# Kernel tuning notes

Hardware: AMD Instinct MI355X
Metric: run time of the kernel (lower is better)

Reference implementation:

```python
import jax, jax.numpy as jnp
import numpy as np

B, T, C, H = 2, 2048, 1024, 16
D = C // H  # head dim = 64
EPS = 1e-6  # kernel adds 1e-6 to softmax denominator


def setup_inputs() -> dict:
    key = jax.random.key(0)
    k1, k2, k3, k4, k5 = jax.random.split(key, 5)
    s = 1.0 / np.sqrt(C)
    return {
        "x": jax.random.normal(k1, (B, T, C), dtype=jnp.float32),
        "w_attn": jax.random.normal(k2, (3 * C, C), dtype=jnp.float32) * s,
        "b_attn": jax.random.normal(k3, (3 * C,), dtype=jnp.float32) * 0.02,
        "w_proj": jax.random.normal(k4, (C, C), dtype=jnp.float32) * s,
        "b_proj": jax.random.normal(k5, (C,), dtype=jnp.float32) * 0.02,
    }


def reference(x, w_attn, b_attn, w_proj, b_proj):
    b, t, c = x.shape
    qkv = x @ w_attn.T + b_attn                      # [B,T,3C]
    q, k, v = jnp.split(qkv, 3, axis=2)
    # [B,T,C] -> [B,H,T,D]
    q = q.reshape(b, t, H, D).transpose(0, 2, 1, 3)
    k = k.reshape(b, t, H, D).transpose(0, 2, 1, 3)
    v = v.reshape(b, t, H, D).transpose(0, 2, 1, 3)
    scale = 1.0 / np.sqrt(D)
    att = jnp.einsum("bhid,bhjd->bhij", q, k) * scale  # [B,H,T,T]
    causal = jnp.tril(jnp.ones((t, t), dtype=bool))
    att = jnp.where(causal, att, -jnp.inf)
    # softmax matching the HIP kernel: denom has +1e-6
    m = jnp.max(att, axis=-1, keepdims=True)
    e = jnp.exp(att - m)                             # masked entries -> 0
    p = e / (jnp.sum(e, axis=-1, keepdims=True) + EPS)
    y = jnp.einsum("bhij,bhjd->bhid", p, v)          # [B,H,T,D]
    y = y.transpose(0, 2, 1, 3).reshape(b, t, c)     # [B,T,C]
    return y @ w_proj.T + b_proj
```

## Files before the change

### kernel.cpp

```cpp
#include <hip/hip_runtime.h>

#define B_ 2
#define T_ 2048
#define C_ 1024
#define H_ 16
#define D_ 64

typedef __bf16 bf16x8 __attribute__((ext_vector_type(8)));
typedef float f32x4 __attribute__((ext_vector_type(4)));

__device__ __forceinline__ unsigned short f2bf(float f) {
  unsigned u = __float_as_uint(f);
  unsigned r = (u + 0x7fffu + ((u >> 16) & 1u)) >> 16;
  return (unsigned short)r;
}

__device__ __forceinline__ float exp2_hw(float x) {
  float r;
  asm("v_exp_f32 %0, %1" : "=v"(r) : "v"(x));
  return r;
}

#define NX 1048576
#define NWA 786432
#define NWP 262144
__global__ __launch_bounds__(256) void convert_all(
    const float* __restrict__ x, const float* __restrict__ wa,
    const float* __restrict__ wp, unsigned short* __restrict__ xb,
    unsigned short* __restrict__ wab, unsigned short* __restrict__ wpb) {
  int i = blockIdx.x * 256 + threadIdx.x;
  const float* s; unsigned short* d; int j;
  if (i < NX)            { s = x;  d = xb;  j = i; }
  else if (i < NX + NWA) { s = wa; d = wab; j = i - NX; }
  else                   { s = wp; d = wpb; j = i - NX - NWA; }
  float4 v = ((const float4*)s)[j];
  ushort4 u;
  u.x = f2bf(v.x); u.y = f2bf(v.y); u.z = f2bf(v.z); u.w = f2bf(v.w);
  ((ushort4*)d)[j] = u;
}

__global__ __launch_bounds__(256) void gemm_bt(
    const unsigned short* __restrict__ A,
    const unsigned short* __restrict__ Bm,
    const float* __restrict__ bias,
    int M, int N, int K, int mode,
    float* __restrict__ outf,
    unsigned short* __restrict__ qb,
    unsigned short* __restrict__ kb,
    unsigned short* __restrict__ vb) {
  __shared__ unsigned short As[128 * 64];
  __shared__ unsigned short Bs[128 * 64];

  const int tid  = threadIdx.x;
  const int lane = tid & 63;
  const int wave = tid >> 6;
  const int quad = lane >> 4;
  const int l16  = lane & 15;
  const int q4   = quad * 4;

  const int bm = blockIdx.y * 128;
  const int bn = blockIdx.x * 128;
  const int wm = (wave >> 1) * 64;
  const int wn = (wave & 1) * 64;

  f32x4 acc[4][4] = {};

  const int srow8 = lane >> 3;
  const int scol  = ((lane & 7) ^ srow8) * 8;
  const int srow  = wave * 8 + srow8;

  for (int k0 = 0; k0 < K; k0 += 64) {
#pragma unroll
    for (int c = 0; c < 4; ++c) {
      const int r = c * 32 + srow;
      const unsigned short* ga = A  + (size_t)(bm + r) * K + (k0 + scol);
      const unsigned short* gb = Bm + (size_t)(bn + r) * K + (k0 + scol);
      unsigned short* la = &As[(c * 32 + wave * 8) * 64];
      unsigned short* lb = &Bs[(c * 32 + wave * 8) * 64];
      __builtin_amdgcn_global_load_lds(
          (__attribute__((address_space(1))) unsigned int*)ga,
          (__attribute__((address_space(3))) unsigned int*)la, 16, 0, 0);
      __builtin_amdgcn_global_load_lds(
          (__attribute__((address_space(1))) unsigned int*)gb,
          (__attribute__((address_space(3))) unsigned int*)lb, 16, 0, 0);
    }
    __syncthreads();
#pragma unroll
    for (int ks = 0; ks < 2; ++ks) {
      bf16x8 af[4], bfr[4];
#pragma unroll
      for (int i = 0; i < 4; ++i)
        af[i] = *(const bf16x8*)&As[(wm + i * 16 + l16) * 64 +
                                    (((ks * 4 + quad) ^ (l16 & 7)) * 8)];
#pragma unroll
      for (int j = 0; j < 4; ++j)
        bfr[j] = *(const bf16x8*)&Bs[(wn + j * 16 + l16) * 64 +
                                     (((ks * 4 + quad) ^ (l16 & 7)) * 8)];
#pragma unroll
      for (int i = 0; i < 4; ++i)
#pragma unroll
        for (int j = 0; j < 4; ++j)
          acc[i][j] = __builtin_amdgcn_mfma_f32_16x16x32_bf16(af[i], bfr[j], acc[i][j], 0, 0, 0);
    }
    __syncthreads();
  }

#pragma unroll
  for (int j = 0; j < 4; ++j) {
    const int gn = bn + wn + j * 16 + l16;
    const float bv = bias[gn];
    if (mode == 0) {
#pragma unroll
      for (int i = 0; i < 4; ++i)
#pragma unroll
        for (int r = 0; r < 4; ++r) {
          const int gm = bm + wm + i * 16 + q4 + r;
          outf[(size_t)gm * N + gn] = acc[i][j][r] + bv;
        }
    } else {
      const int which = gn >> 10;
      const int cc = gn & 1023;
      const int h = cc >> 6, d = cc & 63;
      if (which == 2) {
#pragma unroll
        for (int i = 0; i < 4; ++i) {
          const int gm0 = bm + wm + i * 16 + q4;
          const int b = gm0 >> 11, t0 = gm0 & 2047;
          ushort4 u;
          u.x = f2bf(acc[i][j][0] + bv);
          u.y = f2bf(acc[i][j][1] + bv);
          u.z = f2bf(acc[i][j][2] + bv);
          u.w = f2bf(acc[i][j][3] + bv);
          *(ushort4*)&vb[(((size_t)(b * H_ + h) * D_) + d) * T_ + t0] = u;
        }
      } else {
        const float sc = (which == 0) ? 0.18033688011112042f : 1.0f;
        unsigned short* dst = (which == 0) ? qb : kb;
#pragma unroll
        for (int i = 0; i < 4; ++i)
#pragma unroll
          for (int r = 0; r < 4; ++r) {
            const int gm = bm + wm + i * 16 + q4 + r;
            const int b = gm >> 11, t = gm & 2047;
            dst[(((size_t)(b * H_ + h) * T_) + t) * D_ + d] = f2bf((acc[i][j][r] + bv) * sc);
          }
      }
    }
  }
}

__global__ __launch_bounds__(256, 2) void attn_mfma(
    const unsigned short* __restrict__ Qb,
    const unsigned short* __restrict__ Kb,
    const unsigned short* __restrict__ Vtg,
    unsigned short* __restrict__ Yb,
    unsigned short* __restrict__ op,
    float* __restrict__ lp) {
  __shared__ unsigned short Ks[2][64 * 64];
  __shared__ unsigned short Vt[2][64 * 64];
  __shared__ unsigned short Pw[4][32 * 64];

  const int tid  = threadIdx.x;
  const int lane = tid & 63;
  const int wave = tid >> 6;
  const int quad = lane >> 4;
  const int l16  = lane & 15;
  const int q4   = quad * 4;
  const int sw   = (l16 & 7);

  const int id = blockIdx.x;
  const int bh = id / 40;
  const int w  = id - bh * 40;
  int qt, chunk, nsplits;
  if (w < 4)       { qt = w;                 chunk = 0;            nsplits = 1; }
  else if (w < 12) { qt = 4 + ((w - 4) >> 1); chunk = (w - 4) & 1;  nsplits = 2; }
  else if (w < 24) { qt = 8 + (w - 12) / 3;  chunk = (w - 12) % 3; nsplits = 3; }
  else             { qt = 12 + ((w - 24) >> 2); chunk = (w - 24) & 3; nsplits = 4; }

  const int tiles_total = 2 * qt + 2;
  const int tpc = (tiles_total + nsplits - 1) / nsplits;
  const int t0 = chunk * tpc;
  const int t1 = min(t0 + tpc, tiles_total);

  const int b = bh >> 4, h = bh & 15;
  const size_t base = (size_t)bh * T_ * D_;
  const int wq = qt * 128 + wave * 32;
  const int wt1 = min(t1, (wq + 95) >> 6);

  bf16x8 qf[2][2];
#pragma unroll
  for (int nt = 0; nt < 2; ++nt)
#pragma unroll
    for (int ks = 0; ks < 2; ++ks)
      qf[nt][ks] = *(const bf16x8*)(Qb + base + (size_t)(wq + nt * 16 + l16) * 64 +
                                    ks * 32 + quad * 8);

  f32x4 o[4][2] = {};
  float l2[2] = {0.f, 0.f};

  const int srow8 = lane >> 3;
  const int satom = ((lane & 7) ^ srow8) * 8;

#define STAGE_KV(KT, BI)                                                       \
  do {                                                                         \
    const int kt0s = (KT) * 64;                                                \
    _Pragma("unroll")                                                          \
    for (int c = 0; c < 2; ++c) {                                              \
      const int row = wave * 16 + c * 8 + srow8;                               \
      const unsigned short* gk = Kb + base + (size_t)(kt0s + row) * 64 + satom;\
      const unsigned short* gv = Vtg + base + (size_t)row * T_ + kt0s + satom; \
      unsigned short* lk = &Ks[BI][(wave * 16 + c * 8) * 64];                  \
      unsigned short* lv = &Vt[BI][(wave * 16 + c * 8) * 64];                  \
      __builtin_amdgcn_global_load_lds(                                        \
          (__attribute__((address_space(1))) unsigned int*)gk,                 \
          (__attribute__((address_space(3))) unsigned int*)lk, 16, 0, 0);      \
      __builtin_amdgcn_global_load_lds(                                        \
          (__attribute__((address_space(1))) unsigned int*)gv,                 \
          (__attribute__((address_space(3))) unsigned int*)lv, 16, 0, 0);      \
    }                                                                          \
  } while (0)

  STAGE_KV(t0, 0);
  int cur = 0;

  for (int kt = t0; kt < t1; ++kt) {
    const int kt0 = kt * 64;
    __syncthreads();
    if (kt + 1 < t1) STAGE_KV(kt + 1, cur ^ 1);

    if (kt < wt1) {
      f32x4 s[4][2] = {};
#pragma unroll
      for (int ks = 0; ks < 2; ++ks) {
        bf16x8 kf[4];
#pragma unroll
        for (int mt = 0; mt < 4; ++mt)
          kf[mt] = *(const bf16x8*)&Ks[cur][(mt * 16 + l16) * 64 +
                                           (((ks * 4 + quad) ^ sw) * 8)];
        __builtin_amdgcn_s_setprio(1);
#pragma unroll
        for (int mt = 0; mt < 4; ++mt)
#pragma unroll
          for (int nt = 0; nt < 2; ++nt)
            s[mt][nt] = __builtin_amdgcn_mfma_f32_16x16x32_bf16(kf[mt], qf[nt][ks],
                                                                s[mt][nt], 0, 0, 0);
        __builtin_amdgcn_s_setprio(0);
      }
      if (kt0 + 63 > wq) {
#pragma unroll
        for (int mt = 0; mt < 4; ++mt)
#pragma unroll
          for (int nt = 0; nt < 2; ++nt)
#pragma unroll
            for (int r = 0; r < 4; ++r)
              if (kt0 + mt * 16 + q4 + r > wq + nt * 16 + l16) s[mt][nt][r] = -1e30f;
      }
#pragma unroll
      for (int nt = 0; nt < 2; ++nt) {
        float ps = 0.f;
#pragma unroll
        for (int mt = 0; mt < 4; ++mt) {
          float p0 = exp2_hw(s[mt][nt][0]);
          float p1 = exp2_hw(s[mt][nt][1]);
          float p2 = exp2_hw(s[mt][nt][2]);
          float p3 = exp2_hw(s[mt][nt][3]);
          ps += (p0 + p1) + (p2 + p3);
          unsigned lo, hi;
          asm("v_cvt_pk_bf16_f32 %0, %1, %2" : "=v"(lo) : "v"(p0), "v"(p1));
          asm("v_cvt_pk_bf16_f32 %0, %1, %2" : "=v"(hi) : "v"(p2), "v"(p3));
          uint2 pk; pk.x = lo; pk.y = hi;
          const int atom = (2 * mt + (quad >> 1)) ^ sw;
          *(uint2*)&Pw[wave][(nt * 16 + l16) * 64 + atom * 8 + (quad & 1) * 4] = pk;
        }
        l2[nt] += ps;
      }
#pragma unroll
      for (int ks = 0; ks < 2; ++ks) {
        bf16x8 vf[4], pf[2];
#pragma unroll
        for (int dt = 0; dt < 4; ++dt)
          vf[dt] = *(const bf16x8*)&Vt[cur][(dt * 16 + l16) * 64 +
                                           (((ks * 4 + quad) ^ sw) * 8)];
#pragma unroll
        for (int nt = 0; nt < 2; ++nt)
          pf[nt] = *(const bf16x8*)&Pw[wave][(nt * 16 + l16) * 64 +
                                            (((ks * 4 + quad) ^ sw) * 8)];
        __builtin_amdgcn_s_setprio(1);
#pragma unroll
        for (int dt = 0; dt < 4; ++dt)
#pragma unroll
          for (int nt = 0; nt < 2; ++nt)
            o[dt][nt] = __builtin_amdgcn_mfma_f32_16x16x32_bf16(vf[dt], pf[nt],
                                                                o[dt][nt], 0, 0, 0);
        __builtin_amdgcn_s_setprio(0);
      }
    }
    cur ^= 1;
  }
#undef STAGE_KV

#pragma unroll
  for (int nt = 0; nt < 2; ++nt) {
    float l = l2[nt];
    l += __shfl_xor(l, 16);
    l += __shfl_xor(l, 32);
    const int qloc = wave * 32 + nt * 16 + l16;
    if (nsplits == 1) {
      const float inv = 1.f / (l + 1e-6f);
      const int q = qt * 128 + qloc;
#pragma unroll
      for (int dt = 0; dt < 4; ++dt) {
        ushort4 u;
        u.x = f2bf(o[dt][nt][0] * inv);
        u.y = f2bf(o[dt][nt][1] * inv);
        u.z = f2bf(o[dt][nt][2] * inv);
        u.w = f2bf(o[dt][nt][3] * inv);
        *(ushort4*)&Yb[((size_t)(b * T_ + q)) * C_ + h * 64 + dt * 16 + q4] = u;
      }
    } else {
      if (quad == 0) lp[(size_t)id * 128 + qloc] = l;
#pragma unroll
      for (int dt = 0; dt < 4; ++dt) {
        ushort4 u;
        u.x = f2bf(o[dt][nt][0]);
        u.y = f2bf(o[dt][nt][1]);
        u.z = f2bf(o[dt][nt][2]);
        u.w = f2bf(o[dt][nt][3]);
        *(ushort4*)&op[(size_t)id * 8192 + (size_t)qloc * 64 + dt * 16 + q4] = u;
      }
    }
  }
}

__global__ __launch_bounds__(256) void attn_combine(
    const unsigned short* __restrict__ op, const float* __restrict__ lp,
    unsigned short* __restrict__ Yb) {
  const int cb = blockIdx.x;
  const int bh = cb / 12;
  const int qi = cb - bh * 12;
  const int qt = 4 + qi;
  int nsplits, pfx;
  if (qt < 8)       { nsplits = 2; pfx = 4 + 2 * (qt - 4); }
  else if (qt < 12) { nsplits = 3; pfx = 12 + 3 * (qt - 8); }
  else              { nsplits = 4; pfx = 24 + 4 * (qt - 12); }
  const int slot0 = bh * 40 + pfx;

  const int t = threadIdx.x;
  const int qloc = t >> 1;
  const int d0 = (t & 1) * 32;

  float l = 1e-6f;
  float acc[32];
#pragma unroll
  for (int i = 0; i < 32; ++i) acc[i] = 0.f;
  for (int s = 0; s < nsplits; ++s) {
    l += lp[(size_t)(slot0 + s) * 128 + qloc];
    const uint4* src = (const uint4*)(op + (size_t)(slot0 + s) * 8192 +
                                      (size_t)qloc * 64 + d0);
#pragma unroll
    for (int c = 0; c < 4; ++c) {
      uint4 v = src[c];
      acc[c*8+0] += __uint_as_float(v.x << 16);
      acc[c*8+1] += __uint_as_float(v.x & 0xffff0000u);
      acc[c*8+2] += __uint_as_float(v.y << 16);
      acc[c*8+3] += __uint_as_float(v.y & 0xffff0000u);
      acc[c*8+4] += __uint_as_float(v.z << 16);
      acc[c*8+5] += __uint_as_float(v.z & 0xffff0000u);
      acc[c*8+6] += __uint_as_float(v.w << 16);
      acc[c*8+7] += __uint_as_float(v.w & 0xffff0000u);
    }
  }
  const float inv = 1.f / l;
  const int b = bh >> 4, h = bh & 15;
  const int q = qt * 128 + qloc;
  uint4* dst = (uint4*)(Yb + ((size_t)(b * T_ + q)) * C_ + h * 64 + d0);
#pragma unroll
  for (int c = 0; c < 4; ++c) {
    uint4 v;
    v.x = (unsigned)f2bf(acc[c*8+0] * inv) | ((unsigned)f2bf(acc[c*8+1] * inv) << 16);
    v.y = (unsigned)f2bf(acc[c*8+2] * inv) | ((unsigned)f2bf(acc[c*8+3] * inv) << 16);
    v.z = (unsigned)f2bf(acc[c*8+4] * inv) | ((unsigned)f2bf(acc[c*8+5] * inv) << 16);
    v.w = (unsigned)f2bf(acc[c*8+6] * inv) | ((unsigned)f2bf(acc[c*8+7] * inv) << 16);
    dst[c] = v;
  }
}

extern "C" void kernel_launch(void* const* d_in, const int* in_sizes, int n_in,
                              void* d_out, int out_size, void* d_ws, size_t ws_size,
                              hipStream_t stream) {
  const float* x      = (const float*)d_in[0];
  const float* w_attn = (const float*)d_in[1];
  const float* b_attn = (const float*)d_in[2];
  const float* w_proj = (const float*)d_in[3];
  const float* b_proj = (const float*)d_in[4];
  float* out = (float*)d_out;

  char* ws = (char*)d_ws;
  unsigned short* xb  = (unsigned short*)ws;  ws += (size_t)4096 * 1024 * 2;
  unsigned short* wab = (unsigned short*)ws;  ws += (size_t)3072 * 1024 * 2;
  unsigned short* wpb = (unsigned short*)ws;  ws += (size_t)1024 * 1024 * 2;
  unsigned short* qb  = (unsigned short*)ws;  ws += (size_t)B_ * H_ * T_ * D_ * 2;
  unsigned short* kb  = (unsigned short*)ws;  ws += (size_t)B_ * H_ * T_ * D_ * 2;
  unsigned short* vb  = (unsigned short*)ws;  ws += (size_t)B_ * H_ * T_ * D_ * 2;
  unsigned short* yb  = (unsigned short*)ws;  ws += (size_t)4096 * 1024 * 2;
  unsigned short* op  = (unsigned short*)ws;  ws += (size_t)1280 * 128 * 64 * 2;
  float*          lp  = (float*)ws;           ws += (size_t)1280 * 128 * 4;
  (void)ws_size; (void)in_sizes; (void)n_in; (void)out_size;

  convert_all<<<8192, 256, 0, stream>>>(x, w_attn, w_proj, xb, wab, wpb);

  gemm_bt<<<dim3(24, 32), 256, 0, stream>>>(xb, wab, b_attn, 4096, 3072, 1024, 1,
                                            nullptr, qb, kb, vb);
  attn_mfma<<<1280, 256, 0, stream>>>(qb, kb, vb, yb, op, lp);
  attn_combine<<<384, 256, 0, stream>>>(op, lp, yb);
  gemm_bt<<<dim3(8, 32), 256, 0, stream>>>(yb, wpb, b_proj, 4096, 1024, 1024, 0,
                                           out, nullptr, nullptr, nullptr);
}
```

Baseline: 185.8 us.

## Add 256x256 double-buffered QKV GEMM with direct global-to-LDS loads

Replaces the 128x128 QKV projection GEMM with a dedicated 512-thread kernel that computes 256x256 tiles. It double-buffers LDS, stages tiles with global_load_lds, and splits each K-step into four phases that interleave the next tile's loads with MFMA work, using barriers and priority hints. Blocks are remapped so neighbouring blocks share tiles. The aim is more data reuse per block and less time waiting on loads, but the grid drops to 192 blocks (fewer than the CU count) and each block uses much more LDS and registers, which limits occupancy.

```diff
diff --git a/kernel.cpp b/kernel.cpp
--- a/kernel.cpp
+++ b/kernel.cpp
@@ -39,15 +39,159 @@
   ((ushort4*)d)[j] = u;
 }
 
+__global__ __launch_bounds__(512, 2) void gemm_qkv_256(
+    const unsigned short* __restrict__ A,
+    const unsigned short* __restrict__ Bm,
+    const float* __restrict__ bias,
+    unsigned short* __restrict__ qb,
+    unsigned short* __restrict__ kb,
+    unsigned short* __restrict__ vb) {
+  __shared__ unsigned short As[2][256 * 64];
+  __shared__ unsigned short Bs[2][256 * 64];
+
+  const int tid  = threadIdx.x;
+  const int lane = tid & 63;
+  const int wave = tid >> 6;
+  const int quad = lane >> 4;
+  const int l16  = lane & 15;
+  const int q4   = quad * 4;
+  const int wr   = wave >> 2;
+  const int wc   = wave & 3;
+
+  const int id0 = blockIdx.x;
+  const int nid = (id0 & 7) * 24 + (id0 >> 3);
+  const int bm = (nid / 12) * 256;
+  const int bn = (nid % 12) * 256;
+
+  f32x4 acc[8][4] = {};
+  bf16x8 af[2][4], bf[2][2];
+
+  const int srow8 = lane >> 3;
+  const int satom = ((lane & 7) ^ srow8) * 8;
+
+#define STG64(G, LPTR, GROW, KCOL)                                             \
+  do {                                                                         \
+    const unsigned short* g_ = (G) + (size_t)(GROW) * 1024 + (KCOL) + satom;   \
+    __builtin_amdgcn_global_load_lds(                                          \
+        (__attribute__((address_space(1))) unsigned int*)g_,                   \
+        (__attribute__((address_space(3))) unsigned int*)(LPTR), 16, 0, 0);    \
+  } while (0)
+
+#define STG_HALF(G, LS, BUF, HH, KCOL, RB)                                     \
+  do {                                                                         \
+    STG64(G, &LS[BUF][((HH) * 128 + wave * 8) * 64],                           \
+          (RB) + (HH) * 128 + wave * 8 + srow8, KCOL);                         \
+    STG64(G, &LS[BUF][((HH) * 128 + 64 + wave * 8) * 64],                      \
+          (RB) + (HH) * 128 + 64 + wave * 8 + srow8, KCOL);                    \
+  } while (0)
+
+#define LOAD_AF(BUF, IH)                                                       \
+  _Pragma("unroll") for (int ks_ = 0; ks_ < 2; ++ks_)                          \
+  _Pragma("unroll") for (int i_ = 0; i_ < 4; ++i_)                             \
+    af[ks_][i_] = *(const bf16x8*)&As[BUF][(wr * 128 + (IH) * 64 + i_ * 16 +   \
+                                            l16) * 64 +                        \
+                                           (((ks_ * 4 + quad) ^ (l16 & 7)) * 8)]
+
+#define LOAD_BF(BUF, JH)                                                       \
+  _Pragma("unroll") for (int ks_ = 0; ks_ < 2; ++ks_)                          \
+  _Pragma("unroll") for (int j_ = 0; j_ < 2; ++j_)                             \
+    bf[ks_][j_] = *(const bf16x8*)&Bs[BUF][(wc * 64 + (JH) * 32 + j_ * 16 +    \
+                                            l16) * 64 +                        \
+                                           (((ks_ * 4 + quad) ^ (l16 & 7)) * 8)]
+
+#define MFMA_Q(IH, JH)                                                         \
+  _Pragma("unroll") for (int ks_ = 0; ks_ < 2; ++ks_)                          \
+  _Pragma("unroll") for (int i_ = 0; i_ < 4; ++i_)                             \
+  _Pragma("unroll") for (int j_ = 0; j_ < 2; ++j_)                             \
+    acc[(IH) * 4 + i_][(JH) * 2 + j_] = __builtin_amdgcn_mfma_f32_16x16x32_bf16( \
+        af[ks_][i_], bf[ks_][j_], acc[(IH) * 4 + i_][(JH) * 2 + j_], 0, 0, 0)
+
+#define PHASE(BUF, IH, JH, LA, LB, STGSTMT, DRAIN)                             \
+  do {                                                                         \
+    if (LA) { LOAD_AF(BUF, IH); }                                              \
+    if (LB) { LOAD_BF(BUF, JH); }                                              \
+    STGSTMT;                                                                   \
+    __builtin_amdgcn_s_barrier();                                              \
+    asm volatile("s_waitcnt lgkmcnt(0)" ::: "memory");                         \
+    __builtin_amdgcn_sched_barrier(0);                                         \
+    __builtin_amdgcn_s_setprio(1);                                             \
+    MFMA_Q(IH, JH);                                                            \
+    __builtin_amdgcn_s_setprio(0);                                             \
+    __builtin_amdgcn_sched_barrier(0);                                         \
+    if (DRAIN) asm volatile("s_waitcnt vmcnt(0)" ::: "memory");                \
+    __builtin_amdgcn_s_barrier();                                              \
+  } while (0)
+
+  STG_HALF(A,  As, 0, 0, 0, bm);
+  STG_HALF(A,  As, 0, 1, 0, bm);
+  STG_HALF(Bm, Bs, 0, 0, 0, bn);
+  STG_HALF(Bm, Bs, 0, 1, 0, bn);
+  asm volatile("s_waitcnt vmcnt(0)" ::: "memory");
+  __builtin_amdgcn_s_barrier();
+
+  for (int kt = 0; kt < 15; ++kt) {
+    const int cb = kt & 1, nb = cb ^ 1;
+    const int kn = (kt + 1) * 64;
+    PHASE(cb, 0, 0, 1, 1,
+          { STG_HALF(A, As, nb, 0, kn, bm); STG_HALF(Bm, Bs, nb, 0, kn, bn); }, 0);
+    PHASE(cb, 1, 0, 1, 0,
+          { STG_HALF(A, As, nb, 1, kn, bm); STG_HALF(Bm, Bs, nb, 1, kn, bn); }, 0);
+    PHASE(cb, 1, 1, 0, 1, (void)0, 0);
+    PHASE(cb, 0, 1, 1, 0, (void)0, 1);
+  }
+
+  LOAD_AF(1, 0); LOAD_BF(1, 0); MFMA_Q(0, 0);
+  LOAD_AF(1, 1);                MFMA_Q(1, 0);
+                 LOAD_BF(1, 1); MFMA_Q(1, 1);
+  LOAD_AF(1, 0);                MFMA_Q(0, 1);
+
+#undef PHASE
+#undef MFMA_Q
+#undef LOAD_BF
+#undef LOAD_AF
+#undef STG_HALF
+#undef STG64
+
+#pragma unroll
+  for (int j = 0; j < 4; ++j) {
+    const int gn = bn + wc * 64 + j * 16 + l16;
+    const float bv = bias[gn];
+    const int which = gn >> 10;
+    const int cc = gn & 1023;
+    const int h = cc >> 6, d = cc & 63;
+    if (which == 2) {
+#pragma unroll
+      for (int i = 0; i < 8; ++i) {
+        const int gm0 = bm + wr * 128 + i * 16 + q4;
+        const int b = gm0 >> 11, t0 = gm0 & 2047;
+        ushort4 u;
+        u.x = f2bf(acc[i][j][0] + bv);
+        u.y = f2bf(acc[i][j][1] + bv);
+        u.z = f2bf(acc[i][j][2] + bv);
+        u.w = f2bf(acc[i][j][3] + bv);
+        *(ushort4*)&vb[(((size_t)(b * H_ + h) * D_) + d) * T_ + t0] = u;
+      }
+    } else {
+      const float sc = (which == 0) ? 0.18033688011112042f : 1.0f;
+      unsigned short* dst = (which == 0) ? qb : kb;
+#pragma unroll
+      for (int i = 0; i < 8; ++i)
+#pragma unroll
+        for (int r = 0; r < 4; ++r) {
+          const int gm = bm + wr * 128 + i * 16 + q4 + r;
+          const int b = gm >> 11, t = gm & 2047;
+          dst[(((size_t)(b * H_ + h) * T_) + t) * D_ + d] = f2bf((acc[i][j][r] + bv) * sc);
+        }
+    }
+  }
+}
+
 __global__ __launch_bounds__(256) void gemm_bt(
     const unsigned short* __restrict__ A,
     const unsigned short* __restrict__ Bm,
     const float* __restrict__ bias,
-    int M, int N, int K, int mode,
-    float* __restrict__ outf,
-    unsigned short* __restrict__ qb,
-    unsigned short* __restrict__ kb,
-    unsigned short* __restrict__ vb) {
+    int M, int N, int K,
+    float* __restrict__ outf) {
   __shared__ unsigned short As[128 * 64];
   __shared__ unsigned short Bs[128 * 64];
 
@@ -109,43 +253,13 @@
   for (int j = 0; j < 4; ++j) {
     const int gn = bn + wn + j * 16 + l16;
     const float bv = bias[gn];
-    if (mode == 0) {
-#pragma unroll
-      for (int i = 0; i < 4; ++i)
-#pragma unroll
-        for (int r = 0; r < 4; ++r) {
-          const int gm = bm + wm + i * 16 + q4 + r;
-          outf[(size_t)gm * N + gn] = acc[i][j][r] + bv;
-        }
-    } else {
-      const int which = gn >> 10;
-      const int cc = gn & 1023;
-      const int h = cc >> 6, d = cc & 63;
-      if (which == 2) {
-#pragma unroll
-        for (int i = 0; i < 4; ++i) {
-          const int gm0 = bm + wm + i * 16 + q4;
-          const int b = gm0 >> 11, t0 = gm0 & 2047;
-          ushort4 u;
-          u.x = f2bf(acc[i][j][0] + bv);
-          u.y = f2bf(acc[i][j][1] + bv);
-          u.z = f2bf(acc[i][j][2] + bv);
-          u.w = f2bf(acc[i][j][3] + bv);
-          *(ushort4*)&vb[(((size_t)(b * H_ + h) * D_) + d) * T_ + t0] = u;
-        }
-      } else {
-        const float sc = (which == 0) ? 0.18033688011112042f : 1.0f;
-        unsigned short* dst = (which == 0) ? qb : kb;
-#pragma unroll
-        for (int i = 0; i < 4; ++i)
-#pragma unroll
-          for (int r = 0; r < 4; ++r) {
-            const int gm = bm + wm + i * 16 + q4 + r;
-            const int b = gm >> 11, t = gm & 2047;
-            dst[(((size_t)(b * H_ + h) * T_) + t) * D_ + d] = f2bf((acc[i][j][r] + bv) * sc);
-          }
-      }
-    }
+#pragma unroll
+    for (int i = 0; i < 4; ++i)
+#pragma unroll
+      for (int r = 0; r < 4; ++r) {
+        const int gm = bm + wm + i * 16 + q4 + r;
+        outf[(size_t)gm * N + gn] = acc[i][j][r] + bv;
+      }
   }
 }
 
@@ -409,10 +523,9 @@
 
   convert_all<<<8192, 256, 0, stream>>>(x, w_attn, w_proj, xb, wab, wpb);
 
-  gemm_bt<<<dim3(24, 32), 256, 0, stream>>>(xb, wab, b_attn, 4096, 3072, 1024, 1,
-                                            nullptr, qb, kb, vb);
+  gemm_qkv_256<<<192, 512, 0, stream>>>(xb, wab, b_attn, qb, kb, vb);
   attn_mfma<<<1280, 256, 0, stream>>>(qb, kb, vb, yb, op, lp);
   attn_combine<<<384, 256, 0, stream>>>(op, lp, yb);
-  gemm_bt<<<dim3(8, 32), 256, 0, stream>>>(yb, wpb, b_proj, 4096, 1024, 1024, 0,
-                                           out, nullptr, nullptr, nullptr);
-}
+  gemm_bt<<<dim3(8, 32), 256, 0, stream>>>(yb, wpb, b_proj, 4096, 1024, 1024,
+                                           out);
+}
```

Measured after the change: 189.3 us. No clear change (+1.9%).

## Load K and V fragments directly from global memory, dropping LDS staging

Applied to the files above, without the earlier changes.

Removes the double-buffered LDS staging of K and V tiles (global_load_lds plus a block-wide barrier per tile). Each wave now loads its K and V MFMA fragments straight from global memory into registers and loops only to its own causal limit. This drops the per-tile __syncthreads and frees LDS. In exchange, the four waves each fetch the same K/V data separately, relying on L1/L2 for reuse. There is no prefetch, so global load latency is exposed before the MFMAs.

```diff
diff --git a/kernel.cpp b/kernel.cpp
--- a/kernel.cpp
+++ b/kernel.cpp
@@ -156,8 +156,6 @@
     unsigned short* __restrict__ Yb,
     unsigned short* __restrict__ op,
     float* __restrict__ lp) {
-  __shared__ unsigned short Ks[2][64 * 64];
-  __shared__ unsigned short Vt[2][64 * 64];
   __shared__ unsigned short Pw[4][32 * 64];
 
   const int tid  = threadIdx.x;
@@ -185,7 +183,7 @@
   const int b = bh >> 4, h = bh & 15;
   const size_t base = (size_t)bh * T_ * D_;
   const int wq = qt * 128 + wave * 32;
-  const int wt1 = min(t1, (wq + 95) >> 6);
+  const int wmax = min(t1, (wq + 95) >> 6);
 
   bf16x8 qf[2][2];
 #pragma unroll
@@ -198,106 +196,85 @@
   f32x4 o[4][2] = {};
   float l2[2] = {0.f, 0.f};
 
-  const int srow8 = lane >> 3;
-  const int satom = ((lane & 7) ^ srow8) * 8;
-
-#define STAGE_KV(KT, BI)                                                       \
-  do {                                                                         \
-    const int kt0s = (KT) * 64;                                                \
-    _Pragma("unroll")                                                          \
-    for (int c = 0; c < 2; ++c) {                                              \
-      const int row = wave * 16 + c * 8 + srow8;                               \
-      const unsigned short* gk = Kb + base + (size_t)(kt0s + row) * 64 + satom;\
-      const unsigned short* gv = Vtg + base + (size_t)row * T_ + kt0s + satom; \
-      unsigned short* lk = &Ks[BI][(wave * 16 + c * 8) * 64];                  \
-      unsigned short* lv = &Vt[BI][(wave * 16 + c * 8) * 64];                  \
-      __builtin_amdgcn_global_load_lds(                                        \
-          (__attribute__((address_space(1))) unsigned int*)gk,                 \
-          (__attribute__((address_space(3))) unsigned int*)lk, 16, 0, 0);      \
-      __builtin_amdgcn_global_load_lds(                                        \
-          (__attribute__((address_space(1))) unsigned int*)gv,                 \
-          (__attribute__((address_space(3))) unsigned int*)lv, 16, 0, 0);      \
-    }                                                                          \
-  } while (0)
-
-  STAGE_KV(t0, 0);
-  int cur = 0;
-
-  for (int kt = t0; kt < t1; ++kt) {
+  for (int kt = t0; kt < wmax; ++kt) {
     const int kt0 = kt * 64;
-    __syncthreads();
-    if (kt + 1 < t1) STAGE_KV(kt + 1, cur ^ 1);
-
-    if (kt < wt1) {
-      f32x4 s[4][2] = {};
-#pragma unroll
-      for (int ks = 0; ks < 2; ++ks) {
-        bf16x8 kf[4];
-#pragma unroll
-        for (int mt = 0; mt < 4; ++mt)
-          kf[mt] = *(const bf16x8*)&Ks[cur][(mt * 16 + l16) * 64 +
-                                           (((ks * 4 + quad) ^ sw) * 8)];
-        __builtin_amdgcn_s_setprio(1);
-#pragma unroll
-        for (int mt = 0; mt < 4; ++mt)
-#pragma unroll
-          for (int nt = 0; nt < 2; ++nt)
-            s[mt][nt] = __builtin_amdgcn_mfma_f32_16x16x32_bf16(kf[mt], qf[nt][ks],
-                                                                s[mt][nt], 0, 0, 0);
-        __builtin_amdgcn_s_setprio(0);
+
+    bf16x8 kf[2][4], vf[2][4];
+#pragma unroll
+    for (int ks = 0; ks < 2; ++ks)
+#pragma unroll
+      for (int mt = 0; mt < 4; ++mt)
+        kf[ks][mt] = *(const bf16x8*)(Kb + base +
+                                      (size_t)(kt0 + mt * 16 + l16) * 64 +
+                                      ks * 32 + quad * 8);
+#pragma unroll
+    for (int ks = 0; ks < 2; ++ks)
+#pragma unroll
+      for (int dt = 0; dt < 4; ++dt)
+        vf[ks][dt] = *(const bf16x8*)(Vtg + base +
+                                      (size_t)(dt * 16 + l16) * T_ +
+                                      kt0 + ks * 32 + quad * 8);
+
+    f32x4 s[4][2] = {};
+#pragma unroll
+    for (int ks = 0; ks < 2; ++ks) {
+      __builtin_amdgcn_s_setprio(1);
+#pragma unroll
+      for (int mt = 0; mt < 4; ++mt)
+#pragma unroll
+        for (int nt = 0; nt < 2; ++nt)
+          s[mt][nt] = __builtin_amdgcn_mfma_f32_16x16x32_bf16(kf[ks][mt], qf[nt][ks],
+                                                              s[mt][nt], 0, 0, 0);
+      __builtin_amdgcn_s_setprio(0);
+    }
+
+    if (kt0 + 63 > wq) {
+#pragma unroll
+      for (int mt = 0; mt < 4; ++mt)
+#pragma unroll
+        for (int nt = 0; nt < 2; ++nt)
+#pragma unroll
+          for (int r = 0; r < 4; ++r)
+            if (kt0 + mt * 16 + q4 + r > wq + nt * 16 + l16) s[mt][nt][r] = -1e30f;
+    }
+
+#pragma unroll
+    for (int nt = 0; nt < 2; ++nt) {
+      float ps = 0.f;
+#pragma unroll
+      for (int mt = 0; mt < 4; ++mt) {
+        float p0 = exp2_hw(s[mt][nt][0]);
+        float p1 = exp2_hw(s[mt][nt][1]);
+        float p2 = exp2_hw(s[mt][nt][2]);
+        float p3 = exp2_hw(s[mt][nt][3]);
+        ps += (p0 + p1) + (p2 + p3);
+        unsigned lo, hi;
+        asm("v_cvt_pk_bf16_f32 %0, %1, %2" : "=v"(lo) : "v"(p0), "v"(p1));
+        asm("v_cvt_pk_bf16_f32 %0, %1, %2" : "=v"(hi) : "v"(p2), "v"(p3));
+        uint2 pk; pk.x = lo; pk.y = hi;
+        const int atom = (2 * mt + (quad >> 1)) ^ sw;
+        *(uint2*)&Pw[wave][(nt * 16 + l16) * 64 + atom * 8 + (quad & 1) * 4] = pk;
       }
-      if (kt0 + 63 > wq) {
-#pragma unroll
-        for (int mt = 0; mt < 4; ++mt)
-#pragma unroll
-          for (int nt = 0; nt < 2; ++nt)
-#pragma unroll
-            for (int r = 0; r < 4; ++r)
-              if (kt0 + mt * 16 + q4 + r > wq + nt * 16 + l16) s[mt][nt][r] = -1e30f;
-      }
-#pragma unroll
-      for (int nt = 0; nt < 2; ++nt) {
-        float ps = 0.f;
-#pragma unroll
-        for (int mt = 0; mt < 4; ++mt) {
-          float p0 = exp2_hw(s[mt][nt][0]);
-          float p1 = exp2_hw(s[mt][nt][1]);
-          float p2 = exp2_hw(s[mt][nt][2]);
-          float p3 = exp2_hw(s[mt][nt][3]);
-          ps += (p0 + p1) + (p2 + p3);
-          unsigned lo, hi;
-          asm("v_cvt_pk_bf16_f32 %0, %1, %2" : "=v"(lo) : "v"(p0), "v"(p1));
-          asm("v_cvt_pk_bf16_f32 %0, %1, %2" : "=v"(hi) : "v"(p2), "v"(p3));
-          uint2 pk; pk.x = lo; pk.y = hi;
-          const int atom = (2 * mt + (quad >> 1)) ^ sw;
-          *(uint2*)&Pw[wave][(nt * 16 + l16) * 64 + atom * 8 + (quad & 1) * 4] = pk;
-        }
-        l2[nt] += ps;
-      }
-#pragma unroll
-      for (int ks = 0; ks < 2; ++ks) {
-        bf16x8 vf[4], pf[2];
-#pragma unroll
-        for (int dt = 0; dt < 4; ++dt)
-          vf[dt] = *(const bf16x8*)&Vt[cur][(dt * 16 + l16) * 64 +
-                                           (((ks * 4 + quad) ^ sw) * 8)];
+      l2[nt] += ps;
+    }
+
+#pragma unroll
+    for (int ks = 0; ks < 2; ++ks) {
+      bf16x8 pf[2];
+#pragma unroll
+      for (int nt = 0; nt < 2; ++nt)
+        pf[nt] = *(const bf16x8*)&Pw[wave][(nt * 16 + l16) * 64 +
+                                          (((ks * 4 + quad) ^ sw) * 8)];
+      __builtin_amdgcn_s_setprio(1);
+#pragma unroll
+      for (int dt = 0; dt < 4; ++dt)
 #pragma unroll
         for (int nt = 0; nt < 2; ++nt)
-          pf[nt] = *(const bf16x8*)&Pw[wave][(nt * 16 + l16) * 64 +
-                                            (((ks * 4 + quad) ^ sw) * 8)];
-        __builtin_amdgcn_s_setprio(1);
-#pragma unroll
-        for (int dt = 0; dt < 4; ++dt)
-#pragma unroll
-          for (int nt = 0; nt < 2; ++nt)
-            o[dt][nt] = __builtin_amdgcn_mfma_f32_16x16x32_bf16(vf[dt], pf[nt],
-                                                                o[dt][nt], 0, 0, 0);
-        __builtin_amdgcn_s_setprio(0);
-      }
-    }
-    cur ^= 1;
-  }
-#undef STAGE_KV
+          o[dt][nt] = __builtin_amdgcn_mfma_f32_16x16x32_bf16(vf[ks][dt], pf[nt],
+                                                              o[dt][nt], 0, 0, 0);
+      __builtin_amdgcn_s_setprio(0);
+    }
+  }
 
 #pragma unroll
   for (int nt = 0; nt < 2; ++nt) {
```

Measured after the change: 226.4 us. 21.8% more time.
